# Optimization experiments

Hardware: AMD Instinct MI355X
Metric: run time of the kernel (lower is better)

The kernel has to match this reference:

```python
import jax, jax.numpy as jnp
import numpy as np

NUM_CLASSES = 2
TIME_STEPS = 1000
B = 16
L = 1024


def _cosine_schedule(num_steps, s=0.01):
    # Faithful port of beta_schedule(..., 'cosine') + __init__ log buffers (float64 -> float32).
    t = np.arange(0, num_steps + 1, dtype=np.float64)
    f_t = np.cos((t / num_steps + s) / (1 + s) * np.pi * 0.5) ** 2
    alpha_bars = f_t / f_t[0]
    alphas = np.clip(alpha_bars[1:] / alpha_bars[:-1], 0.001, 0.999)
    alphas = np.sqrt(alphas)
    log_alphas = np.log(alphas)
    log_alpha_bars = np.cumsum(log_alphas)
    log_1_minus_alphas = np.log(1.0 - np.exp(log_alphas) + 1e-40)
    log_1_minus_alpha_bars = np.log(1.0 - np.exp(log_alpha_bars) + 1e-40)
    f32 = lambda x: jnp.asarray(x, jnp.float32)
    return f32(log_alphas), f32(log_1_minus_alphas), f32(log_alpha_bars), f32(log_1_minus_alpha_bars)


def setup_inputs() -> dict:
    key = jax.random.key(0)
    k1, k2, k3 = jax.random.split(key, 3)
    # log_x_t: log one-hot, as produced by log_sample_categorical (clamp min 1e-30 -> log)
    x_t = jax.random.randint(k1, (B, 1, L, L), 0, NUM_CLASSES)
    onehot = jax.nn.one_hot(x_t, NUM_CLASSES, axis=1, dtype=jnp.float32)  # (B,K,1,L,L)
    log_x_t = jnp.log(jnp.clip(onehot, 1e-30))
    # log_x_0: log-softmax distribution, as produced by predict_x_0 (F.log_softmax over class dim)
    logits0 = jax.random.normal(k2, (B, NUM_CLASSES, 1, L, L), jnp.float32)
    log_x_0 = jax.nn.log_softmax(logits0, axis=1)
    la, l1a, lab, l1ab = _cosine_schedule(TIME_STEPS)
    t = jax.random.randint(k3, (B,), 0, TIME_STEPS).astype(jnp.int64)
    return {
        'log_x_t': log_x_t,
        'log_x_0': log_x_0,
        'log_alphas': la,
        'log_1_minus_alphas': l1a,
        'log_alpha_bars': lab,
        'log_1_minus_alpha_bars': l1ab,
        't': t,
    }


def reference(log_x_t, log_x_0, log_alphas, log_1_minus_alphas, log_alpha_bars, log_1_minus_alpha_bars, t):
    # MultinomialDiffusion.q_posterior: gather(extract) + log_add_exp + where-mask + logsumexp over class dim.
    K = log_x_0.shape[1]
    log_K = jnp.log(jnp.asarray(K, log_x_0.dtype))
    ext = lambda a, tt: a[tt].reshape(-1, 1, 1, 1, 1)  # extract(a, t, x_shape)

    # q_pred(log_x_0, t-1) with t-1 clamped to 0
    t_m1 = jnp.maximum(t - 1, 0)
    log_EV_qxtmin_x0 = jnp.logaddexp(
        log_x_0 + ext(log_alpha_bars, t_m1),
        ext(log_1_minus_alpha_bars, t_m1) - log_K,
    )
    # where t == 0, posterior mean is log_x_0 itself
    t_b = t.reshape(-1, 1, 1, 1, 1)
    log_EV_qxtmin_x0 = jnp.where(t_b == 0, log_x_0, log_EV_qxtmin_x0)

    # q_pred_one_step(log_x_t, t)
    log_one_step = jnp.logaddexp(
        log_x_t + ext(log_alphas, t),
        ext(log_1_minus_alphas, t) - log_K,
    )

    unnormed = log_EV_qxtmin_x0 + log_one_step
    return unnormed - jax.nn.logsumexp(unnormed, axis=1, keepdims=True)
```

## Files before the change

### kernel.cpp

```cpp
#include <hip/hip_runtime.h>


#define LL (1024 * 1024)
#define BLOCKS_PER_B 256
#define ITER 4
#define STRIDE (BLOCKS_PER_B * 256)

typedef float vfloat4 __attribute__((ext_vector_type(4)));

__global__ __launch_bounds__(256) void qposterior_kernel(
    const float* __restrict__ lxt,
    const float* __restrict__ lx0,
    const float* __restrict__ la,
    const float* __restrict__ l1a,
    const float* __restrict__ lab,
    const float* __restrict__ l1ab,
    const int* __restrict__ tarr,
    float* __restrict__ out)
{
    const float LOGK = 0.6931471805599453f;

    int bid   = blockIdx.x;
    int b     = bid >> 8;
    int local = bid & (BLOCKS_PER_B - 1);

    int tb = tarr[b];
    bool t0 = (tb == 0);
    float C = la[tb];
    float D = l1a[tb] - LOGK;
    float mm = fmaxf(C, D);
    float s_hot = mm + __logf(1.0f + __expf(fminf(C, D) - mm));
    float delta = s_hot - D;

    float a = 0.f, c = 0.f, apc = 0.f;
    if (!t0) {
        int tm1 = tb - 1;
        a   = __expf(lab[tm1]);
        c   = 0.5f * __expf(l1ab[tm1]);
        apc = a + c;
    }

    const float* xt_p  = lxt + b * (2 * LL);
    const float* x0_p  = lx0 + b * (2 * LL);
    float*       out_p = out + b * (2 * LL);

    int g0 = local * 256 + threadIdx.x;

#pragma unroll
    for (int it = 0; it < ITER; ++it) {
        int e = (g0 + it * STRIDE) * 4;

        vfloat4 xt = *reinterpret_cast<const vfloat4*>(xt_p + e);
        vfloat4 x0 = *reinterpret_cast<const vfloat4*>(x0_p + e);
        vfloat4 x1 = {0.f, 0.f, 0.f, 0.f};
        if (t0) x1 = *reinterpret_cast<const vfloat4*>(x0_p + e + LL);

        vfloat4 r0, r1;
#pragma unroll
        for (int i = 0; i < 4; ++i) {
            float l00 = x0[i];
            float d;
            if (t0) {
                d = l00 - x1[i];
            } else {
                float p  = __expf(l00);
                float e0 = __logf(fmaf(a, p, c));
                float e1 = __logf(fmaf(-a, p, apc));
                d = e0 - e1;
            }
            float sd    = (xt[i] > -35.0f) ? delta : -delta;
            float Delta = d + sd;
            float m  = fmaxf(-Delta, 0.0f);
            float o0 = -(m + __logf(1.0f + __expf(-fabsf(Delta))));
            r0[i] = o0;
            r1[i] = o0 - Delta;
        }

        __builtin_nontemporal_store(r0, reinterpret_cast<vfloat4*>(out_p + e));
        __builtin_nontemporal_store(r1, reinterpret_cast<vfloat4*>(out_p + e + LL));
    }
}

extern "C" void kernel_launch(void* const* d_in, const int* in_sizes, int n_in,
                              void* d_out, int out_size, void* d_ws, size_t ws_size,
                              hipStream_t stream) {
    const float* lxt  = (const float*)d_in[0];
    const float* lx0  = (const float*)d_in[1];
    const float* la   = (const float*)d_in[2];
    const float* l1a  = (const float*)d_in[3];
    const float* lab  = (const float*)d_in[4];
    const float* l1ab = (const float*)d_in[5];
    const int*   tarr = (const int*)d_in[6];
    float*       out  = (float*)d_out;

    const int grid  = 16 * BLOCKS_PER_B;
    const int block = 256;

    qposterior_kernel<<<grid, block, 0, stream>>>(lxt, lx0, la, l1a, lab, l1ab, tarr, out);
}
```

Baseline: 290.8 us.

## Use a flat grid-stride loop, simplify the posterior algebra, and use plain stores

Replaces the per-batch block mapping with a flat grid-stride loop over all batches using 2048 blocks and 8 iterations per thread. The t>0 path is rewritten algebraically: the normalisation becomes three logs (u, v, w) with precomputed exp(±delta) instead of two logs plus a softplus. Per-batch scalars are now reloaded and recomputed every iteration. Nontemporal stores are replaced by regular stores. The kernel stays memory-bound, so the fewer transcendentals may matter little, while the redundant scalar work and the change of store type could cost something.

```diff
diff --git a/kernel.cpp b/kernel.cpp
--- a/kernel.cpp
+++ b/kernel.cpp
@@ -2,9 +2,11 @@
 
 
 #define LL (1024 * 1024)
-#define BLOCKS_PER_B 256
-#define ITER 4
-#define STRIDE (BLOCKS_PER_B * 256)
+#define GROUPS_PER_PLANE (1 << 18)
+#define NBLOCKS 2048
+#define NTHREADS 256
+#define GSTRIDE (NBLOCKS * NTHREADS)
+#define NITER ((16 * GROUPS_PER_PLANE) / GSTRIDE)
 
 typedef float vfloat4 __attribute__((ext_vector_type(4)));
 
@@ -20,64 +22,66 @@
 {
     const float LOGK = 0.6931471805599453f;
 
-    int bid   = blockIdx.x;
-    int b     = bid >> 8;
-    int local = bid & (BLOCKS_PER_B - 1);
+    int g = blockIdx.x * NTHREADS + threadIdx.x;
 
-    int tb = tarr[b];
-    bool t0 = (tb == 0);
-    float C = la[tb];
-    float D = l1a[tb] - LOGK;
-    float mm = fmaxf(C, D);
-    float s_hot = mm + __logf(1.0f + __expf(fminf(C, D) - mm));
-    float delta = s_hot - D;
+#pragma unroll 2
+    for (int it = 0; it < NITER; ++it, g += GSTRIDE) {
+        int b  = g >> 18;
+        int eg = (g & (GROUPS_PER_PLANE - 1)) << 2;
 
-    float a = 0.f, c = 0.f, apc = 0.f;
-    if (!t0) {
-        int tm1 = tb - 1;
-        a   = __expf(lab[tm1]);
-        c   = 0.5f * __expf(l1ab[tm1]);
-        apc = a + c;
-    }
+        const float* xt_p  = lxt + b * (2 * LL) + eg;
+        const float* x0_p  = lx0 + b * (2 * LL) + eg;
+        float*       out_p = out + b * (2 * LL) + eg;
 
-    const float* xt_p  = lxt + b * (2 * LL);
-    const float* x0_p  = lx0 + b * (2 * LL);
-    float*       out_p = out + b * (2 * LL);
+        vfloat4 xt4 = *reinterpret_cast<const vfloat4*>(xt_p);
+        vfloat4 x04 = *reinterpret_cast<const vfloat4*>(x0_p);
 
-    int g0 = local * 256 + threadIdx.x;
-
-#pragma unroll
-    for (int it = 0; it < ITER; ++it) {
-        int e = (g0 + it * STRIDE) * 4;
-
-        vfloat4 xt = *reinterpret_cast<const vfloat4*>(xt_p + e);
-        vfloat4 x0 = *reinterpret_cast<const vfloat4*>(x0_p + e);
-        vfloat4 x1 = {0.f, 0.f, 0.f, 0.f};
-        if (t0) x1 = *reinterpret_cast<const vfloat4*>(x0_p + e + LL);
+        int tb = tarr[b];
+        float C = la[tb];
+        float D = l1a[tb] - LOGK;
+        float mm = fmaxf(C, D);
+        float s_hot = mm + __logf(1.0f + __expf(fminf(C, D) - mm));
+        float delta = s_hot - D;
 
         vfloat4 r0, r1;
+        if (tb != 0) {
+            int tm1 = tb - 1;
+            float a   = __expf(lab[tm1]);
+            float c   = 0.5f * __expf(l1ab[tm1]);
+            float apc = a + c;
+            float Fp  = __expf(delta);
+            float Fm  = __expf(-delta);
 #pragma unroll
-        for (int i = 0; i < 4; ++i) {
-            float l00 = x0[i];
-            float d;
-            if (t0) {
-                d = l00 - x1[i];
-            } else {
-                float p  = __expf(l00);
-                float e0 = __logf(fmaf(a, p, c));
-                float e1 = __logf(fmaf(-a, p, apc));
-                d = e0 - e1;
+            for (int i = 0; i < 4; ++i) {
+                float p  = __expf(x04[i]);
+                float u  = fmaf(a, p, c);
+                float v  = fmaf(-a, p, apc);
+                bool hot = (xt4[i] > -35.0f);
+                float F  = hot ? Fp : Fm;
+                float sd = hot ? delta : -delta;
+                float w  = fmaf(u, F, v);
+                float lu = __logf(u);
+                float lv = __logf(v);
+                float lw = __logf(w);
+                r0[i] = (lu - lw) + sd;
+                r1[i] = lv - lw;
             }
-            float sd    = (xt[i] > -35.0f) ? delta : -delta;
-            float Delta = d + sd;
-            float m  = fmaxf(-Delta, 0.0f);
-            float o0 = -(m + __logf(1.0f + __expf(-fabsf(Delta))));
-            r0[i] = o0;
-            r1[i] = o0 - Delta;
+        } else {
+            vfloat4 x14 = *reinterpret_cast<const vfloat4*>(x0_p + LL);
+#pragma unroll
+            for (int i = 0; i < 4; ++i) {
+                float d     = x04[i] - x14[i];
+                float sd    = (xt4[i] > -35.0f) ? delta : -delta;
+                float Delta = d + sd;
+                float m  = fmaxf(-Delta, 0.0f);
+                float o0 = -(m + __logf(1.0f + __expf(-fabsf(Delta))));
+                r0[i] = o0;
+                r1[i] = o0 - Delta;
+            }
         }
 
-        __builtin_nontemporal_store(r0, reinterpret_cast<vfloat4*>(out_p + e));
-        __builtin_nontemporal_store(r1, reinterpret_cast<vfloat4*>(out_p + e + LL));
+        *reinterpret_cast<vfloat4*>(out_p)      = r0;
+        *reinterpret_cast<vfloat4*>(out_p + LL) = r1;
     }
 }
 
@@ -93,8 +97,5 @@
     const int*   tarr = (const int*)d_in[6];
     float*       out  = (float*)d_out;
 
-    const int grid  = 16 * BLOCKS_PER_B;
-    const int block = 256;
-
-    qposterior_kernel<<<grid, block, 0, stream>>>(lxt, lx0, la, l1a, lab, l1ab, tarr, out);
+    qposterior_kernel<<<NBLOCKS, NTHREADS, 0, stream>>>(lxt, lx0, la, l1a, lab, l1ab, tarr, out);
 }
```

After: 293.6 us. About the same (+1.0%).
